# Performance work log

Measured on AMD Instinct MI355X. Metric: run time of the kernel, lower is better.

The kernel has to match this reference:

```python
import jax, jax.numpy as jnp
import numpy as np

ANG = 7; C = 32; H = 32; W = 32; B = 4
E = 4 * C; HEADS = 4; NV = ANG * 32; TOK = C * NV; HID = int(C * 2.66)


def _ln(x, g, b, eps=1e-6):
    m = x.mean(-1, keepdims=True)
    v = ((x - m) ** 2).mean(-1, keepdims=True)
    return (x - m) * jax.lax.rsqrt(v + eps) * g + b


def _ln_nchw(x, g, b):
    return _ln(x.transpose(0, 2, 3, 1), g, b).transpose(0, 3, 1, 2)


def _l2(x):
    return x / jnp.maximum(jnp.linalg.norm(x, axis=-1, keepdims=True), 1e-12)


def _c11(w, x):  # 1x1 conv, w: [out, in]
    return jnp.einsum('oc,bchw->bohw', w, x)


def _dw3(x, w):  # depthwise 3x3, w: [Ch, 1, 3, 3]
    return jax.lax.conv_general_dilated(x, w, (1, 1), ((1, 1), (1, 1)),
                                        dimension_numbers=('NCHW', 'OIHW', 'NCHW'),
                                        feature_group_count=x.shape[1])


def _branch(buf, p):  # buf: [B, C, N, V, W]
    lin_w, temp, ln1_g, ln1_b, qkv_w, qkvdw_w, proj_w, attca_w, lne_g, lne_b, pin_w, dw_w, pout_w = p
    Bb, Cc, N, V, Wd = buf.shape
    L = V * Wd
    x_tok = buf.transpose(0, 3, 4, 1, 2).reshape(Bb, L, Cc * N) @ lin_w.T  # [B, L, E]
    x_res = buf.transpose(0, 2, 1, 3, 4).reshape(Bb * N, Cc, V, Wd)
    x = x_tok.reshape(Bb, V, Wd, E).transpose(0, 3, 1, 2)  # [B, E, V, W]
    qkv = _dw3(_c11(qkv_w, _ln_nchw(x, ln1_g, ln1_b)), qkvdw_w)
    q, k, v_ = jnp.split(qkv, 3, axis=1)
    d = E // HEADS
    to_heads = lambda t: t.reshape(Bb, HEADS, d, L).transpose(0, 1, 3, 2)  # [B, h, L, d]
    q, k, v_ = _l2(to_heads(q)), _l2(to_heads(k)), to_heads(v_)
    logits = jnp.einsum('bhld,bhmd->bhlm', q, k) * temp
    attn0 = jax.nn.softmax(logits, axis=-1)
    a1 = jnp.maximum(logits, 0.0) ** 2
    a1 = jax.nn.gelu(a1, approximate=False) * a1
    scale, shift = jnp.split(jnp.einsum('oh,bhlm->bolm', attca_w, a1), 2, axis=1)
    attn = attn0 * (1.0 + scale) + shift
    out = jnp.einsum('bhlm,bhmd->bhld', attn, v_).transpose(0, 1, 3, 2).reshape(Bb, E, V, Wd)
    out = _c11(proj_w, out).reshape(Bb, Cc, N, V, Wd).transpose(0, 2, 1, 3, 4).reshape(Bb * N, Cc, V, Wd)
    x = x_res + out
    h2 = _dw3(_c11(pin_w, _ln_nchw(x, lne_g, lne_b)), dw_w)
    h1, hg = jnp.split(h2, 2, axis=1)
    x = x + _c11(pout_w, jax.nn.gelu(h1, approximate=False) * hg)
    return x.reshape(Bb, N, Cc, V, Wd).transpose(0, 2, 1, 3, 4)


def _forward(x_lf, hp, vp, f1_w, f2_w):
    Bt = x_lf.shape[0]
    Bb = Bt // (ANG * ANG)
    x6 = x_lf.reshape(Bb, ANG, ANG, C, H, W)  # (b,u,v,c,h,w)
    epi1 = x6.transpose(0, 3, 2, 5, 1, 4).reshape(Bb, C, ANG * W, ANG, H)  # b c (v w) u h
    epi2 = x6.transpose(0, 3, 1, 4, 2, 5).reshape(Bb, C, ANG * H, ANG, W)  # b c (u h) v w
    o1 = _branch(epi1, hp).reshape(Bb, C, ANG, W, ANG, H).transpose(0, 4, 2, 1, 5, 3).reshape(Bt, C, H, W)
    o2 = _branch(epi2, vp).reshape(Bb, C, ANG, H, ANG, W).transpose(0, 2, 4, 1, 3, 5).reshape(Bt, C, H, W)
    g = jnp.concatenate([o1, o2], axis=1).max(axis=(2, 3))  # AdaptiveMaxPool2d(1) -> [Bt, 2C]
    g = g @ f1_w.T
    g = jnp.where(g >= 0, g, 0.1 * g)  # LeakyReLU(0.1)
    g = jax.nn.sigmoid(g @ f2_w.T)[:, :, None, None]
    return o1 * g + o2 * (1.0 - g)


def setup_inputs() -> dict:
    key = jax.random.key(0)
    ks = iter(jax.random.split(key, 64))
    rn = lambda shape: jax.random.normal(next(ks), shape, jnp.float32) * 0.02
    d = {"x_lf": jax.random.normal(next(ks), (B * ANG * ANG, C, H, W), jnp.float32)}
    for pref in ("h_", "v_"):
        d[pref + "lin_w"] = rn((E, TOK))
        d[pref + "temp"] = jnp.ones((1, HEADS, 1, 1), jnp.float32)
        d[pref + "ln1_g"] = jnp.ones((E,), jnp.float32)
        d[pref + "ln1_b"] = jnp.zeros((E,), jnp.float32)
        d[pref + "qkv_w"] = rn((3 * E, E))
        d[pref + "qkvdw_w"] = rn((3 * E, 1, 3, 3))
        d[pref + "proj_w"] = rn((TOK, E))
        d[pref + "attca_w"] = rn((2 * HEADS, HEADS))
        d[pref + "lne_g"] = jnp.ones((C,), jnp.float32)
        d[pref + "lne_b"] = jnp.zeros((C,), jnp.float32)
        d[pref + "pin_w"] = rn((2 * HID, C))
        d[pref + "dw_w"] = rn((2 * HID, 1, 3, 3))
        d[pref + "pout_w"] = rn((C, HID))
    d["f1_w"] = rn((C // 4, 2 * C))
    d["f2_w"] = rn((C, C // 4))
    return d


def reference(x_lf, h_lin_w, h_temp, h_ln1_g, h_ln1_b, h_qkv_w, h_qkvdw_w, h_proj_w, h_attca_w,
              h_lne_g, h_lne_b, h_pin_w, h_dw_w, h_pout_w,
              v_lin_w, v_temp, v_ln1_g, v_ln1_b, v_qkv_w, v_qkvdw_w, v_proj_w, v_attca_w,
              v_lne_g, v_lne_b, v_pin_w, v_dw_w, v_pout_w, f1_w, f2_w):
    hp = (h_lin_w, h_temp, h_ln1_g, h_ln1_b, h_qkv_w, h_qkvdw_w, h_proj_w, h_attca_w,
          h_lne_g, h_lne_b, h_pin_w, h_dw_w, h_pout_w)
    vp = (v_lin_w, v_temp, v_ln1_g, v_ln1_b, v_qkv_w, v_qkvdw_w, v_proj_w, v_attca_w,
          v_lne_g, v_lne_b, v_pin_w, v_dw_w, v_pout_w)
    return _forward(x_lf, hp, vp, f1_w, f2_w)
```

## Files before the change

kernel.cpp:

```cpp
#include <hip/hip_runtime.h>
#include <math.h>

typedef unsigned short u16;
typedef unsigned int   u32;
typedef __attribute__((ext_vector_type(8))) short short8;
typedef __attribute__((ext_vector_type(4))) short short4v;
typedef __attribute__((ext_vector_type(4))) float float4v;
typedef __attribute__((ext_vector_type(2))) float float2v;
typedef __attribute__((ext_vector_type(2))) unsigned int u32x2;

#define DI __device__ __forceinline__

DI float b2f(u16 v){ return __uint_as_float(((u32)v) << 16); }
DI u16 f2b(float f){
  u32 u = __float_as_uint(f);
  u32 r = (u + 0x7fffu + ((u >> 16) & 1u)) >> 16;
  return (u16)r;
}
DI float fast_gelu(float x){
  float ax = fabsf(x) * 0.70710678118654752f;
  float t  = __builtin_amdgcn_rcpf(fmaf(0.3275911f, ax, 1.0f));
  float p  = t * (0.254829592f + t * (-0.284496736f + t * (1.421413741f +
             t * (-1.453152027f + t * 1.061405429f))));
  float e  = __expf(-ax * ax);
  float ea = fmaf(-p, e, 1.0f);
  float er = (x >= 0.f) ? ea : -ea;
  return 0.5f * x * (1.0f + er);
}

DI float2v pk_fma(float2v a, float2v b, float2v c){
  float2v d;
  asm("v_pk_fma_f32 %0, %1, %2, %3" : "=v"(d) : "v"(a), "v"(b), "v"(c));
  return d;
}
DI u32 cvt_pk_bf16(float lo, float hi){
  u32 r;
  asm("v_cvt_pk_bf16_f32 %0, %1, %2" : "=v"(r) : "v"(lo), "v"(hi));
  return r;
}


__global__ __launch_bounds__(256) void k_wprep(const float* __restrict__ lw0,
    const float* __restrict__ lw1, const float* __restrict__ pw0,
    const float* __restrict__ pw1, u16* __restrict__ linwB, u16* __restrict__ projB)
{
  int base = blockIdx.x * 1024 + threadIdx.x;
  #pragma unroll
  for (int r = 0; r < 4; ++r) {
    int i = base + 256 * r;
    if (i < 1835008) {
      const float* src = (i < 917504) ? lw0 : lw1;
      linwB[i] = f2b(src[i % 917504]);
    } else if (i < 3670016) {
      int j = i - 1835008;
      const float* src = (j < 917504) ? pw0 : pw1;
      projB[j] = f2b(src[j % 917504]);
    }
  }
}

__global__ __launch_bounds__(256) void k8w_prep(const float* __restrict__ pin0,
    const float* __restrict__ pin1, const float* __restrict__ po0,
    const float* __restrict__ po1, const float* __restrict__ qw0,
    const float* __restrict__ qw1, u16* __restrict__ pinB, u16* __restrict__ poB,
    u16* __restrict__ qkvwB)
{
  int idx = blockIdx.x * 256 + threadIdx.x;
  if (idx < 12288) {
    int cc = idx & 31;
    int r = (idx >> 5) % 96;
    int hb = (idx >> 5) / 96;
    int br = hb >> 1, half = hb & 1;
    const float* p = br ? pin1 : pin0;
    pinB[idx] = (r < 85) ? f2b(p[(half * 85 + r) * 32 + cc]) : (u16)0;
  } else if (idx < 18432) {
    int j = idx - 12288;
    int r = j % 96;
    int t = j / 96;
    int br = t >> 5, cc = t & 31;
    const float* p = br ? po1 : po0;
    poB[j] = (r < 85) ? f2b(p[cc * 85 + r]) : (u16)0;
  } else if (idx < 116736) {
    int j = idx - 18432;
    int br = j / 49152, rest = j % 49152;
    qkvwB[j] = f2b((br ? qw1 : qw0)[rest]);
  }
}

__global__ __launch_bounds__(256) void k1_mfma(const float* __restrict__ xlf,
    const u16* __restrict__ linwB, float* __restrict__ xqp)
{
  __shared__ __align__(16) u16 Asb[64][40];
  __shared__ __align__(16) u16 Wsb[128][40];
  const int ks   = blockIdx.x;
  const int mblk = blockIdx.y;
  const int bb   = blockIdx.z;
  const int br = bb >> 2, b = bb & 3;
  const int tid = threadIdx.x;
  const int wid = tid >> 6, lane = tid & 63;
  const int quad = lane >> 4, r16 = lane & 15;
  const int m0s = mblk * 64 + wid * 16;
  const bool active = (m0s < 224);
  const u16* wsrc = linwB + br * 917504;
  const int c = ks;

  float4v acc[8];
  #pragma unroll
  for (int nt = 0; nt < 8; ++nt) acc[nt] = (float4v){0.f, 0.f, 0.f, 0.f};

  #pragma unroll 1
  for (int step = 0; step < 7; ++step) {
    const int k0 = ks * 224 + step * 32;
    #pragma unroll
    for (int r = 0; r < 2; ++r) {
      int idx = tid + 256 * r;
      if (br == 0) {
        int ml = idx >> 3, kl4 = idx & 7;
        int l = mblk * 64 + ml;
        float4v v4 = {0.f, 0.f, 0.f, 0.f};
        if (l < 224) {
          int u = l >> 5, h = l & 31;
          v4 = *(const float4v*)&xlf[(b * 49 + u * 7 + step) * 32768 + c * 1024 + h * 32 + kl4 * 4];
        }
        u32 lo = cvt_pk_bf16(v4[0], v4[1]);
        u32 hi = cvt_pk_bf16(v4[2], v4[3]);
        *(u32x2*)&Asb[ml][kl4 * 4] = (u32x2){lo, hi};
      } else {
        int ml4 = idx & 15, kl = idx >> 4;
        int ml0 = ml4 * 4;
        int l0 = mblk * 64 + ml0;
        float4v v4 = {0.f, 0.f, 0.f, 0.f};
        if (l0 < 224) {
          int v2 = l0 >> 5, w2 = l0 & 31;
          v4 = *(const float4v*)&xlf[(b * 49 + step * 7 + v2) * 32768 + c * 1024 + kl * 32 + w2];
        }
        Asb[ml0 + 0][kl] = f2b(v4[0]);
        Asb[ml0 + 1][kl] = f2b(v4[1]);
        Asb[ml0 + 2][kl] = f2b(v4[2]);
        Asb[ml0 + 3][kl] = f2b(v4[3]);
      }
    }
    #pragma unroll
    for (int r = 0; r < 4; ++r) {
      int idx = tid + 256 * r;
      int e = idx >> 3, kl4 = idx & 7;
      *(short4v*)&Wsb[e][kl4 * 4] = *(const short4v*)&wsrc[e * 7168 + k0 + kl4 * 4];
    }
    __syncthreads();
    if (active) {
      short8 af = *(const short8*)&Asb[wid * 16 + r16][quad * 8];
      #pragma unroll
      for (int nt = 0; nt < 8; ++nt) {
        short8 bf = *(const short8*)&Wsb[nt * 16 + r16][quad * 8];
        acc[nt] = __builtin_amdgcn_mfma_f32_16x16x32_bf16(af, bf, acc[nt], 0, 0, 0);
      }
    }
    __syncthreads();
  }
  if (active) {
    float* outp = xqp + ks * 229376 + (bb * 224 + m0s) * 128;
    #pragma unroll
    for (int nt = 0; nt < 8; ++nt) {
      int e = nt * 16 + r16;
      #pragma unroll
      for (int reg = 0; reg < 4; ++reg) {
        int tok = quad * 4 + reg;
        outp[tok * 128 + e] = acc[nt][reg];
      }
    }
  }
}

__global__ __launch_bounds__(256) void k1b_ln(const float* __restrict__ xqp,
    const float* __restrict__ g0, const float* __restrict__ b0,
    const float* __restrict__ g1, const float* __restrict__ b1,
    u16* __restrict__ xn)
{
  const int tid = threadIdx.x;
  const int row = blockIdx.x * 16 + (tid >> 4);
  const int p = tid & 15;
  const int bb = row / 224;
  const int br = bb >> 2;
  const float* lg = br ? g1 : g0;
  const float* lb = br ? b1 : b0;
  const int e0 = p * 8;
  float4v a0 = {0.f,0.f,0.f,0.f}, a1 = {0.f,0.f,0.f,0.f};
  const float* src = xqp + row * 128 + e0;
  #pragma unroll
  for (int ks = 0; ks < 32; ++ks) {
    const float4v* sp = (const float4v*)(src + ks * 229376);
    a0 += sp[0];
    a1 += sp[1];
  }
  float s = 0.f, s2 = 0.f;
  #pragma unroll
  for (int j = 0; j < 4; ++j) {
    s  += a0[j] + a1[j];
    s2 += a0[j] * a0[j] + a1[j] * a1[j];
  }
  #pragma unroll
  for (int m = 8; m >= 1; m >>= 1) {
    s  += __shfl_xor(s, m);
    s2 += __shfl_xor(s2, m);
  }
  float mean = s * (1.f / 128.f);
  float var  = s2 * (1.f / 128.f) - mean * mean;
  float rs   = rsqrtf(fmaxf(var, 0.f) + 1e-6f);
  u16 o[8];
  #pragma unroll
  for (int j = 0; j < 4; ++j) {
    o[j]     = f2b((a0[j] - mean) * rs * lg[e0 + j]     + lb[e0 + j]);
    o[4 + j] = f2b((a1[j] - mean) * rs * lg[e0 + 4 + j] + lb[e0 + 4 + j]);
  }
  *(short8*)&xn[row * 128 + e0] = *(const short8*)o;
}

__global__ __launch_bounds__(256) void k3_mfma(const u16* __restrict__ xn,
    const u16* __restrict__ qkvwB, float* __restrict__ qkvp)
{
  __shared__ u16 xnb[112][140];
  const int mchunk = blockIdx.x;
  const int nh = blockIdx.y;
  const int bb = blockIdx.z;
  const int br = bb >> 2;
  const int tid = threadIdx.x;
  const int wid = tid >> 6, lane = tid & 63;
  const int quad = lane >> 4, r16 = lane & 15;

  #pragma unroll
  for (int i = 0; i < 7; ++i) {
    int idx = tid + 256 * i;
    int row = idx >> 4, c8 = idx & 15;
    *(short8*)&xnb[row][c8 * 8] = *(const short8*)&xn[(bb * 224 + nh * 112 + row) * 128 + c8 * 8];
  }
  __syncthreads();

  const int mtile = mchunk * 64 + wid * 16;
  const u16* wsrc = qkvwB + br * 49152;
  float4v acc[7];
  #pragma unroll
  for (int nt = 0; nt < 7; ++nt) acc[nt] = (float4v){0.f, 0.f, 0.f, 0.f};
  #pragma unroll
  for (int k = 0; k < 4; ++k) {
    short8 af = *(const short8*)&wsrc[(mtile + r16) * 128 + k * 32 + quad * 8];
    #pragma unroll
    for (int nt = 0; nt < 7; ++nt) {
      short8 bf = *(const short8*)&xnb[nt * 16 + r16][k * 32 + quad * 8];
      acc[nt] = __builtin_amdgcn_mfma_f32_16x16x32_bf16(af, bf, acc[nt], 0, 0, 0);
    }
  }
  #pragma unroll
  for (int nt = 0; nt < 7; ++nt) {
    int tok = nh * 112 + nt * 16 + r16;
    #pragma unroll
    for (int reg = 0; reg < 4; ++reg) {
      int o = mtile + quad * 4 + reg;
      qkvp[(bb * 384 + o) * 224 + tok] = acc[nt][reg];
    }
  }
}

__global__ __launch_bounds__(256) void k45_dwheads(const float* __restrict__ qkvp,
    const float* __restrict__ dw0, const float* __restrict__ dw1,
    float* __restrict__ qkvn)
{
  __shared__ float ps[32][161];
  __shared__ float ts[32][137];
  __shared__ float scs[128];
  const int bid = blockIdx.x;
  const int half = bid & 1;
  const int rest = bid >> 1;
  const int h = rest & 3;
  const int sel = (rest >> 2) % 3;
  const int bb = rest / 12;
  const int br = bb >> 2;
  const int tid = threadIdx.x;
  const int o0 = sel * 128 + h * 32;
  const float* src = qkvp + (bb * 384 + o0) * 224;
  const float* dwa = (br ? dw1 : dw0) + o0 * 9;
  const int vin0  = half ? 3 : 0;
  const int nin   = half ? 128 : 160;
  const int vout0 = half ? 4 : 0;
  const int nout  = half ? 96 : 128;
  const int lout0 = vout0 * 32;
  for (int idx = tid; idx < 32 * nin; idx += 256) {
    int d = idx / nin, l = idx - d * nin;
    ps[d][l] = src[d * 224 + vin0 * 32 + l];
  }
  __syncthreads();
  for (int idx = tid; idx < 32 * nout; idx += 256) {
    int d = idx / nout, lo = idx - d * nout;
    int l = lout0 + lo;
    int v = l >> 5, w = l & 31;
    const float* dww = dwa + d * 9;
    float acc = 0.f;
    #pragma unroll
    for (int dy = -1; dy <= 1; ++dy) {
      int vv = v + dy; if (vv < 0 || vv > 6) continue;
      int vloc = vv - vin0;
      #pragma unroll
      for (int dx = -1; dx <= 1; ++dx) {
        int ww = w + dx; if (ww < 0 || ww > 31) continue;
        acc += ps[d][vloc * 32 + ww] * dww[(dy + 1) * 3 + (dx + 1)];
      }
    }
    ts[d][lo] = acc;
  }
  __syncthreads();
  if (tid < nout) {
    float ss = 0.f;
    #pragma unroll 8
    for (int d = 0; d < 32; ++d) { float x = ts[d][tid]; ss += x * x; }
    scs[tid] = (sel < 2) ? (1.0f / fmaxf(sqrtf(ss), 1e-12f)) : 1.0f;
  }
  __syncthreads();
  float* dst = qkvn + ((bb * 3 + sel) * 4 + h) * 7168;
  for (int idx = tid; idx < 32 * nout; idx += 256) {
    int d = idx & 31, lo = idx >> 5;
    dst[(lout0 + lo) * 32 + d] = ts[d][lo] * scs[lo];
  }
}

__global__ __launch_bounds__(256) void k6_attn(const float* __restrict__ qkvn,
    const float* __restrict__ tmp0, const float* __restrict__ tmp1,
    const float* __restrict__ ca0,  const float* __restrict__ ca1,
    u16* __restrict__ aoB)
{
  __shared__ float qs[16][33];
  __shared__ float ks[128][33];
  __shared__ float sS[16 * 228];
  __shared__ float mxs[16], rss[16];
  __shared__ float caf[32], tpf[4];
  const int it = blockIdx.x;
  const int b = blockIdx.y, br = blockIdx.z;
  const int bb = br * 4 + b;
  const int tid = threadIdx.x;
  const float* tw = br ? tmp1 : tmp0;
  const float* cw = br ? ca1 : ca0;
  if (tid < 32) caf[tid] = cw[tid];
  if (tid < 4)  tpf[tid] = tw[tid];
  const int i0 = it * 4;
  const float* qb = qkvn + (bb * 3 + 0) * 4 * 7168;
  const float* kb = qkvn + (bb * 3 + 1) * 4 * 7168;
  const float* vb = qkvn + (bb * 3 + 2) * 4 * 7168;
  #pragma unroll
  for (int r = 0; r < 2; ++r) {
    int idx = tid + 256 * r;
    if (idx < 512) {
      int d = idx & 31, i = (idx >> 5) & 3, h = idx >> 7;
      qs[h * 4 + i][d] = qb[h * 7168 + (i0 + i) * 32 + d];
    }
  }
  __syncthreads();
  const int hC = tid >> 6, iC = (tid >> 4) & 3, jq = tid & 15;
  float qv[32];
  #pragma unroll
  for (int d2 = 0; d2 < 32; ++d2) qv[d2] = qs[hC * 4 + iC][d2];
  for (int jt = 0; jt < 7; ++jt) {
    __syncthreads();
    #pragma unroll
    for (int r = 0; r < 16; ++r) {
      int idx = tid + 256 * r;
      int d = idx & 31, jj = (idx >> 5) & 31, h = idx >> 10;
      ks[h * 32 + jj][d] = kb[h * 7168 + (jt * 32 + jj) * 32 + d];
    }
    __syncthreads();
    float a2[2] = {0.f, 0.f};
    for (int d = 0; d < 32; ++d) {
      #pragma unroll
      for (int r = 0; r < 2; ++r) a2[r] += qv[d] * ks[hC * 32 + jq + 16 * r][d];
    }
    #pragma unroll
    for (int r = 0; r < 2; ++r)
      sS[(hC * 4 + iC) * 228 + jt * 32 + jq + 16 * r] = a2[r] * tpf[hC];
  }
  __syncthreads();
  {
    int p = tid & 15, row = tid >> 4;
    float mx = -1e30f;
    for (int q = 0; q < 14; ++q) mx = fmaxf(mx, sS[row * 228 + p + 16 * q]);
    #pragma unroll
    for (int m = 8; m >= 1; m >>= 1) mx = fmaxf(mx, __shfl_xor(mx, m));
    float es = 0.f;
    for (int q = 0; q < 14; ++q) es += __expf(sS[row * 228 + p + 16 * q] - mx);
    #pragma unroll
    for (int m = 8; m >= 1; m >>= 1) es += __shfl_xor(es, m);
    if (p == 0) { mxs[row] = mx; rss[row] = 1.0f / es; }
  }
  __syncthreads();
  for (int q = 0; q < 4; ++q) {
    int pr = tid + 256 * q;
    if (pr < 896) {
      int i = pr / 224, j = pr % 224;
      float a1[4];
      #pragma unroll
      for (int hh = 0; hh < 4; ++hh) {
        float sv = sS[(hh * 4 + i) * 228 + j];
        float z = fmaxf(sv, 0.f); float z2 = z * z;
        a1[hh] = fast_gelu(z2) * z2;
      }
      #pragma unroll
      for (int hh = 0; hh < 4; ++hh) {
        float sc = 0.f, sh = 0.f;
        #pragma unroll
        for (int k2 = 0; k2 < 4; ++k2) { sc += caf[hh * 4 + k2] * a1[k2]; sh += caf[(hh + 4) * 4 + k2] * a1[k2]; }
        int row = hh * 4 + i;
        float at = __expf(sS[row * 228 + j] - mxs[row]) * rss[row];
        sS[row * 228 + j] = at * (1.f + sc) + sh;
      }
    }
  }
  __syncthreads();
  {
    int d = tid & 31, hpair = (tid >> 5) & 1, rg = tid >> 6;
    float acc[2] = {0.f, 0.f};
    for (int jt = 0; jt < 7; ++jt) {
      __syncthreads();
      #pragma unroll
      for (int r = 0; r < 16; ++r) {
        int idx = tid + 256 * r;
        int dd = idx & 31, jj = (idx >> 5) & 31, hh2 = idx >> 10;
        ks[hh2 * 32 + jj][dd] = vb[hh2 * 7168 + (jt * 32 + jj) * 32 + dd];
      }
      __syncthreads();
      for (int j = 0; j < 32; ++j) {
        #pragma unroll
        for (int c2 = 0; c2 < 2; ++c2) {
          int hh = hpair * 2 + c2;
          acc[c2] += sS[(hh * 4 + rg) * 228 + jt * 32 + j] * ks[hh * 32 + j][d];
        }
      }
    }
    #pragma unroll
    for (int c2 = 0; c2 < 2; ++c2) {
      int hh = hpair * 2 + c2;
      aoB[(bb * 224 + i0 + rg) * 128 + hh * 32 + d] = f2b(acc[c2]);
    }
  }
}

__global__ __launch_bounds__(256) void k7_mfma(const u16* __restrict__ aoB,
    const u16* __restrict__ projB, const float* __restrict__ xlf, u16* __restrict__ x2)
{
  __shared__ u16 Bs[224][140];
  __shared__ float Ts[64][68];
  const int mchunk = blockIdx.x;
  const int mi = blockIdx.y;
  const int bb = blockIdx.z;
  const int br = bb >> 2, b = bb & 3;
  const int tid = threadIdx.x;
  const int wid = tid >> 6, lane = tid & 63;
  const int quad = lane >> 4, r16 = lane & 15;
  const u16* asrc = projB + br * 917504;
  #pragma unroll
  for (int i = 0; i < 14; ++i) {
    int idx = tid + 256 * i;
    int row = idx >> 4, c8 = idx & 15;
    *(short8*)&Bs[row][c8 * 8] = *(const short8*)&aoB[(bb * 224 + row) * 128 + c8 * 8];
  }
  __syncthreads();
  const int mbase = mchunk * 256 + (wid * 4 + mi) * 16;
  float4v acc[14];
  #pragma unroll
  for (int nt = 0; nt < 14; ++nt) acc[nt] = (float4v){0.f, 0.f, 0.f, 0.f};
  #pragma unroll
  for (int k = 0; k < 4; ++k) {
    short8 af = *(const short8*)&asrc[(mbase + r16) * 128 + k * 32 + quad * 8];
    #pragma unroll
    for (int nt = 0; nt < 14; ++nt) {
      short8 bf = *(const short8*)&Bs[nt * 16 + r16][k * 32 + quad * 8];
      acc[nt] = __builtin_amdgcn_mfma_f32_16x16x32_bf16(af, bf, acc[nt], 0, 0, 0);
    }
  }
  #pragma unroll
  for (int rd = 0; rd < 4; ++rd) {
    const int ntn = (rd < 3) ? 4 : 2;
    __syncthreads();
    #pragma unroll
    for (int t = 0; t < 4; ++t) {
      if (t < ntn) {
        #pragma unroll
        for (int reg = 0; reg < 4; ++reg)
          Ts[wid * 16 + quad * 4 + reg][t * 16 + r16] = acc[rd * 4 + t][reg];
      }
    }
    __syncthreads();
    const int nq = ntn * 4;
    #pragma unroll
    for (int pass = 0; pass < 4; ++pass) {
      int idx = tid + 256 * pass;
      if (idx < 64 * nq) {
        int rloc = idx / nq;
        int qc = idx - rloc * nq;
        int row = mchunk * 256 + (((rloc >> 4) * 4 + mi) << 4) + (rloc & 15);
        int c = row / 224, n = row - c * 224;
        int l = rd * 64 + qc * 4;
        float4v tv = *(const float4v*)&Ts[rloc][qc * 4];
        float r0v, r1v, r2v, r3v;
        if (br == 0) {
          int img = b * 49 + (l >> 5) * 7 + (n >> 5);
          const float* xp = xlf + img * 32768 + c * 1024 + (l & 31) * 32 + (n & 31);
          r0v = xp[0]; r1v = xp[32]; r2v = xp[64]; r3v = xp[96];
        } else {
          int img = b * 49 + (n >> 5) * 7 + (l >> 5);
          float4v xv = *(const float4v*)(xlf + img * 32768 + c * 1024 + (n & 31) * 32 + (l & 31));
          r0v = xv[0]; r1v = xv[1]; r2v = xv[2]; r3v = xv[3];
        }
        u32 lo = cvt_pk_bf16(tv[0] + r0v, tv[1] + r1v);
        u32 hi = cvt_pk_bf16(tv[2] + r2v, tv[3] + r3v);
        u16* dp = &x2[(((br * 896 + b * 224 + n) * 32 + c) << 8) + l];
        *(u32x2*)dp = (u32x2){lo, hi};
      }
    }
  }
}

__global__ __launch_bounds__(256, 4) void k8_mfma(u16* x2,
    const float* __restrict__ lg0, const float* __restrict__ lb0,
    const float* __restrict__ lg1, const float* __restrict__ lb1,
    const float* __restrict__ dwa0, const float* __restrict__ dwa1,
    const u16* __restrict__ pinB, const u16* __restrict__ poB)
{
  __shared__ __align__(16) u16 xnb[224][36];
  __shared__ __align__(16) u32 t12[16][231];
  __shared__ __align__(16) u16 gsb[224][20];
  const int img = blockIdx.x;
  const int br  = blockIdx.y;
  const float* lg  = br ? lg1 : lg0;
  const float* lb  = br ? lb1 : lb0;
  const float* dww = br ? dwa1 : dwa0;
  const u16* pinBr = pinB + br * 2 * 96 * 32;
  const u16* poBr  = poB + br * 32 * 96;
  const int tid = threadIdx.x;
  const int wid = tid >> 6, lane = tid & 63;
  const int quad = lane >> 4, r16 = lane & 15;
  u16* src = x2 + (br * 896 + img) * 8192;

  if (tid < 224) {
    float xr[32];
    #pragma unroll
    for (int cc = 0; cc < 32; ++cc) xr[cc] = b2f(src[cc * 256 + tid]);
    float s = 0.f, s2 = 0.f;
    #pragma unroll
    for (int cc = 0; cc < 32; ++cc) { s += xr[cc]; s2 += xr[cc] * xr[cc]; }
    float mean = s * (1.f / 32.f);
    float var  = s2 * (1.f / 32.f) - mean * mean;
    float rs   = rsqrtf(fmaxf(var, 0.f) + 1e-6f);
    #pragma unroll
    for (int cc = 0; cc < 32; ++cc)
      xnb[tid][cc] = f2b((xr[cc] - mean) * rs * lg[cc] + lb[cc]);
  }
  __syncthreads();

  float4v acc[7];
  #pragma unroll
  for (int i = 0; i < 7; ++i) acc[i] = (float4v){0.f, 0.f, 0.f, 0.f};

  #pragma unroll 1
  for (int it = 0; it < 6; ++it) {
    const int r0 = it * 16;
    #pragma unroll
    for (int ni = 0; ni < 4; ++ni) {
      int n = wid + 4 * ni;
      if (n < 14) {
        const int tok = n * 16 + r16;
        short8 bf;
        const u16* xp = &xnb[tok][quad * 8];
        ((short4v*)&bf)[0] = *(const short4v*)xp;
        ((short4v*)&bf)[1] = *(const short4v*)(xp + 4);
        short8 af0 = *(const short8*)&pinBr[((r0 + r16) << 5) + quad * 8];
        short8 af1 = *(const short8*)&pinBr[((96 + r0 + r16) << 5) + quad * 8];
        float4v d0 = __builtin_amdgcn_mfma_f32_16x16x32_bf16(af0, bf,
                       (float4v){0.f, 0.f, 0.f, 0.f}, 0, 0, 0);
        float4v d1 = __builtin_amdgcn_mfma_f32_16x16x32_bf16(af1, bf,
                       (float4v){0.f, 0.f, 0.f, 0.f}, 0, 0, 0);
        const int col = tok + (tok >> 5);
        #pragma unroll
        for (int reg = 0; reg < 4; ++reg)
          t12[quad * 4 + reg][col] = cvt_pk_bf16(d0[reg], d1[reg]);
      }
    }
    if (it > 0) {
      const int koff = (it - 1) * 16;
      #pragma unroll
      for (int i = 0; i < 7; ++i) {
        int u = wid + 4 * i;
        int mt = u / 14, n = u - mt * 14;
        short8 af = {}, bf = {};
        if (quad < 2) {
          af = *(const short8*)&poBr[(mt * 16 + r16) * 96 + koff + quad * 8];
          const u16* gp = &gsb[n * 16 + r16][quad * 8];
          ((short4v*)&bf)[0] = *(const short4v*)gp;
          ((short4v*)&bf)[1] = *(const short4v*)(gp + 4);
        }
        acc[i] = __builtin_amdgcn_mfma_f32_16x16x32_bf16(af, bf, acc[i], 0, 0, 0);
      }
    }
    __syncthreads();
    if (tid < 224) {
      const int rl = tid & 15;
      const int v  = tid >> 5;
      const int wh = (tid >> 4) & 1;
      const int r  = r0 + rl;
      float2v wp[9];
      if (r < 85) {
        const float* w1 = dww + r * 9;
        const float* w2 = dww + (85 + r) * 9;
        #pragma unroll
        for (int t = 0; t < 9; ++t) wp[t] = (float2v){w1[t], w2[t]};
      } else {
        #pragma unroll
        for (int t = 0; t < 9; ++t) wp[t] = (float2v){0.f, 0.f};
      }
      const u32* trow = &t12[rl][0];
      const int c0 = v * 33;
      const int base = wh << 4;
      const bool vok0 = (v > 0), vok2 = (v < 6);
      float2v accP = {0.f, 0.f}, accC = {0.f, 0.f}, accN = {0.f, 0.f};
      #pragma unroll
      for (int it2 = 0; it2 < 18; ++it2) {
        bool cok = true;
        if (it2 == 0)  cok = (wh == 1);
        if (it2 == 17) cok = (wh == 0);
        if (cok) {
          const int cw = base - 1 + it2;
          u32 p0 = vok0 ? trow[c0 - 33 + cw] : 0u;
          u32 p1 =        trow[c0 + cw];
          u32 p2 = vok2 ? trow[c0 + 33 + cw] : 0u;
          float2v x0 = {__uint_as_float(p0 << 16), __uint_as_float(p0 & 0xffff0000u)};
          float2v x1 = {__uint_as_float(p1 << 16), __uint_as_float(p1 & 0xffff0000u)};
          float2v x2v = {__uint_as_float(p2 << 16), __uint_as_float(p2 & 0xffff0000u)};
          accP = pk_fma(x0, wp[2], accP);
          accC = pk_fma(x0, wp[1], accC);
          accN = pk_fma(x0, wp[0], accN);
          accP = pk_fma(x1, wp[5], accP);
          accC = pk_fma(x1, wp[4], accC);
          accN = pk_fma(x1, wp[3], accN);
          accP = pk_fma(x2v, wp[8], accP);
          accC = pk_fma(x2v, wp[7], accC);
          accN = pk_fma(x2v, wp[6], accN);
        }
        if (it2 >= 2) {
          float g = fast_gelu(accP[0]) * accP[1];
          gsb[(v << 5) + base + (it2 - 2)][rl] = f2b(g);
        }
        accP = accC; accC = accN; accN = (float2v){0.f, 0.f};
      }
    }
    __syncthreads();
  }
  {
    const int koff = 80;
    #pragma unroll
    for (int i = 0; i < 7; ++i) {
      int u = wid + 4 * i;
      int mt = u / 14, n = u - mt * 14;
      short8 af = {}, bf = {};
      if (quad < 2) {
        af = *(const short8*)&poBr[(mt * 16 + r16) * 96 + koff + quad * 8];
        const u16* gp = &gsb[n * 16 + r16][quad * 8];
        ((short4v*)&bf)[0] = *(const short4v*)gp;
        ((short4v*)&bf)[1] = *(const short4v*)(gp + 4);
      }
      acc[i] = __builtin_amdgcn_mfma_f32_16x16x32_bf16(af, bf, acc[i], 0, 0, 0);
    }
  }
  #pragma unroll
  for (int i = 0; i < 7; ++i) {
    int u = wid + 4 * i;
    int mt = u / 14, n = u - mt * 14;
    #pragma unroll
    for (int reg = 0; reg < 4; ++reg) {
      int cc = mt * 16 + quad * 4 + reg;
      int tok = n * 16 + r16;
      int o = cc * 256 + tok;
      src[o] = f2b(b2f(src[o]) + acc[i][reg]);
    }
  }
}

__global__ __launch_bounds__(256) void k9_pool(const u16* __restrict__ x3, float* __restrict__ gmax)
{
  __shared__ float red[4];
  const int bid = blockIdx.x;
  const int c64 = bid & 63;
  const int t = bid >> 6;
  const int c = c64 & 31, which = c64 >> 5;
  const int b = t / 49; const int uv = t % 49; const int u = uv / 7; const int vq = uv % 7;
  const int tid = threadIdx.x;
  float mx = -1e30f;
  if (which == 0) {
    int h = tid & 31, w0 = tid >> 5;
    #pragma unroll
    for (int r = 0; r < 4; ++r) {
      int w = w0 + 8 * r;
      mx = fmaxf(mx, b2f(x3[((b * 224 + vq * 32 + w) * 32 + c) * 256 + u * 32 + h]));
    }
  } else {
    int w = tid & 31, h0 = tid >> 5;
    #pragma unroll
    for (int r = 0; r < 4; ++r) {
      int h = h0 + 8 * r;
      mx = fmaxf(mx, b2f(x3[((896 + b * 224 + u * 32 + h) * 32 + c) * 256 + vq * 32 + w]));
    }
  }
  #pragma unroll
  for (int m = 32; m >= 1; m >>= 1) mx = fmaxf(mx, __shfl_xor(mx, m));
  if ((tid & 63) == 0) red[tid >> 6] = mx;
  __syncthreads();
  if (tid == 0)
    gmax[t * 64 + c64] = fmaxf(fmaxf(red[0], red[1]), fmaxf(red[2], red[3]));
}

__global__ __launch_bounds__(256) void k9_fc(const float* __restrict__ gmax,
    const float* __restrict__ f1, const float* __restrict__ f2, float* __restrict__ gate)
{
  int t = blockIdx.x * 256 + threadIdx.x;
  if (t >= 196) return;
  float g1[8];
  #pragma unroll
  for (int o = 0; o < 8; ++o) {
    float a = 0.f;
    #pragma unroll
    for (int c2 = 0; c2 < 64; ++c2) a += f1[o * 64 + c2] * gmax[t * 64 + c2];
    g1[o] = (a >= 0.f) ? a : 0.1f * a;
  }
  #pragma unroll
  for (int c2 = 0; c2 < 32; ++c2) {
    float a = 0.f;
    #pragma unroll
    for (int o = 0; o < 8; ++o) a += f2[c2 * 8 + o] * g1[o];
    gate[t * 32 + c2] = 1.f / (1.f + expf(-a));
  }
}

__global__ __launch_bounds__(256) void k9_final(const u16* __restrict__ x3,
    const float* __restrict__ gate, float* __restrict__ out)
{
  __shared__ float o1s[32][33];
  const int bid = blockIdx.x;
  const int c = bid & 31;
  const int t = bid >> 5;
  const int b = t / 49; const int uv = t % 49; const int u = uv / 7; const int vq = uv % 7;
  const int tid = threadIdx.x;
  const float g = gate[t * 32 + c];
  #pragma unroll
  for (int r = 0; r < 4; ++r) {
    int h = tid & 31; int w = (tid >> 5) + 8 * r;
    o1s[w][h] = b2f(x3[((b * 224 + vq * 32 + w) * 32 + c) * 256 + u * 32 + h]);
  }
  __syncthreads();
  #pragma unroll
  for (int r = 0; r < 4; ++r) {
    int w = tid & 31; int h = (tid >> 5) + 8 * r;
    float o2 = b2f(x3[((896 + b * 224 + u * 32 + h) * 32 + c) * 256 + vq * 32 + w]);
    float o1 = o1s[w][h];
    out[(t * 32 + c) * 1024 + h * 32 + w] = o1 * g + o2 * (1.f - g);
  }
}

extern "C" void kernel_launch(void* const* d_in, const int* in_sizes, int n_in,
                              void* d_out, int out_size, void* d_ws, size_t ws_size,
                              hipStream_t stream)
{
  const float* xlf    = (const float*)d_in[0];
  const float* h_lin  = (const float*)d_in[1];
  const float* h_temp = (const float*)d_in[2];
  const float* h_g1   = (const float*)d_in[3];
  const float* h_b1   = (const float*)d_in[4];
  const float* h_qkv  = (const float*)d_in[5];
  const float* h_qdw  = (const float*)d_in[6];
  const float* h_proj = (const float*)d_in[7];
  const float* h_ca   = (const float*)d_in[8];
  const float* h_ge   = (const float*)d_in[9];
  const float* h_be   = (const float*)d_in[10];
  const float* h_pin  = (const float*)d_in[11];
  const float* h_dw   = (const float*)d_in[12];
  const float* h_po   = (const float*)d_in[13];
  const float* v_lin  = (const float*)d_in[14];
  const float* v_temp = (const float*)d_in[15];
  const float* v_g1   = (const float*)d_in[16];
  const float* v_b1   = (const float*)d_in[17];
  const float* v_qkv  = (const float*)d_in[18];
  const float* v_qdw  = (const float*)d_in[19];
  const float* v_proj = (const float*)d_in[20];
  const float* v_ca   = (const float*)d_in[21];
  const float* v_ge   = (const float*)d_in[22];
  const float* v_be   = (const float*)d_in[23];
  const float* v_pin  = (const float*)d_in[24];
  const float* v_dw   = (const float*)d_in[25];
  const float* v_po   = (const float*)d_in[26];
  const float* f1     = (const float*)d_in[27];
  const float* f2     = (const float*)d_in[28];

  char* w = (char*)d_ws;
  u16*   x2    = (u16*)  (w + 0);
  float* xqp   = (float*)(w + 0);
  float* qkvp  = (float*)(w + 29360128);
  float* qkvn  = (float*)(w + 32112640);
  float* gmax  = (float*)(w + 34865152);
  float* gate  = (float*)(w + 34915328);
  u16*   pinB  = (u16*)  (w + 34940416);
  u16*   poB   = (u16*)  (w + 34964992);
  u16*   qkvwB = (u16*)  (w + 34977280);
  u16*   aoB   = (u16*)  (w + 35173888);
  u16*   linwB = (u16*)  (w + 35632640);
  u16*   projB = (u16*)  (w + 39302656);
  u16*   xn    = (u16*)  (w + 42972672);

  k_wprep  <<<3584, 256, 0, stream>>>(h_lin, v_lin, h_proj, v_proj, linwB, projB);
  k8w_prep <<<456, 256, 0, stream>>>(h_pin, v_pin, h_po, v_po, h_qkv, v_qkv, pinB, poB, qkvwB);
  k1_mfma  <<<dim3(32, 4, 8), 256, 0, stream>>>(xlf, linwB, xqp);
  k1b_ln   <<<112, 256, 0, stream>>>(xqp, h_g1, h_b1, v_g1, v_b1, xn);
  k3_mfma  <<<dim3(6, 2, 8), 256, 0, stream>>>(xn, qkvwB, qkvp);
  k45_dwheads <<<192, 256, 0, stream>>>(qkvp, h_qdw, v_qdw, qkvn);
  k6_attn  <<<dim3(56, 4, 2), 256, 0, stream>>>(qkvn, h_temp, v_temp, h_ca, v_ca, aoB);
  k7_mfma  <<<dim3(28, 4, 8), 256, 0, stream>>>(aoB, projB, xlf, x2);
  k8_mfma  <<<dim3(896, 2), 256, 0, stream>>>(x2, h_ge, h_be, v_ge, v_be,
                                              h_dw, v_dw, pinB, poB);
  k9_pool  <<<12544, 256, 0, stream>>>(x2, gmax);
  k9_fc    <<<1, 256, 0, stream>>>(gmax, f1, f2, gate);
  k9_final <<<6272, 256, 0, stream>>>(x2, gate, (float*)d_out);
}
```

Before: 396.9 us.

## Merge weight-prep kernels, fold gate FC into final kernel, drop LDS staging

Combines the two weight-conversion kernels into a single launch and folds the tiny gate FC kernel into the final blend kernel, so each block computes its own gate. Two launches are removed. In the qkv and projection GEMMs, the shared-memory staging of the B operand is removed and fragments are read directly from global memory, which eliminates a barrier and LDS traffic. The cost is that the FC work is repeated in every final block, and the direct global B reads rely on cache hits instead of reuse from LDS.

```diff
diff --git a/kernel.cpp b/kernel.cpp
--- a/kernel.cpp
+++ b/kernel.cpp
@@ -40,50 +40,50 @@
 }
 
 
-__global__ __launch_bounds__(256) void k_wprep(const float* __restrict__ lw0,
+__global__ __launch_bounds__(256) void k_prep(const float* __restrict__ lw0,
     const float* __restrict__ lw1, const float* __restrict__ pw0,
-    const float* __restrict__ pw1, u16* __restrict__ linwB, u16* __restrict__ projB)
-{
-  int base = blockIdx.x * 1024 + threadIdx.x;
-  #pragma unroll
-  for (int r = 0; r < 4; ++r) {
-    int i = base + 256 * r;
-    if (i < 1835008) {
-      const float* src = (i < 917504) ? lw0 : lw1;
-      linwB[i] = f2b(src[i % 917504]);
-    } else if (i < 3670016) {
-      int j = i - 1835008;
-      const float* src = (j < 917504) ? pw0 : pw1;
-      projB[j] = f2b(src[j % 917504]);
-    }
-  }
-}
-
-__global__ __launch_bounds__(256) void k8w_prep(const float* __restrict__ pin0,
-    const float* __restrict__ pin1, const float* __restrict__ po0,
-    const float* __restrict__ po1, const float* __restrict__ qw0,
-    const float* __restrict__ qw1, u16* __restrict__ pinB, u16* __restrict__ poB,
-    u16* __restrict__ qkvwB)
-{
-  int idx = blockIdx.x * 256 + threadIdx.x;
-  if (idx < 12288) {
-    int cc = idx & 31;
-    int r = (idx >> 5) % 96;
-    int hb = (idx >> 5) / 96;
-    int br = hb >> 1, half = hb & 1;
-    const float* p = br ? pin1 : pin0;
-    pinB[idx] = (r < 85) ? f2b(p[(half * 85 + r) * 32 + cc]) : (u16)0;
-  } else if (idx < 18432) {
-    int j = idx - 12288;
-    int r = j % 96;
-    int t = j / 96;
-    int br = t >> 5, cc = t & 31;
-    const float* p = br ? po1 : po0;
-    poB[j] = (r < 85) ? f2b(p[cc * 85 + r]) : (u16)0;
-  } else if (idx < 116736) {
-    int j = idx - 18432;
-    int br = j / 49152, rest = j % 49152;
-    qkvwB[j] = f2b((br ? qw1 : qw0)[rest]);
+    const float* __restrict__ pw1,
+    const float* __restrict__ pin0, const float* __restrict__ pin1,
+    const float* __restrict__ po0,  const float* __restrict__ po1,
+    const float* __restrict__ qw0,  const float* __restrict__ qw1,
+    u16* __restrict__ linwB, u16* __restrict__ projB,
+    u16* __restrict__ pinB, u16* __restrict__ poB, u16* __restrict__ qkvwB)
+{
+  if (blockIdx.x < 3584) {
+    int base = blockIdx.x * 1024 + threadIdx.x;
+    #pragma unroll
+    for (int r = 0; r < 4; ++r) {
+      int i = base + 256 * r;
+      if (i < 1835008) {
+        const float* src = (i < 917504) ? lw0 : lw1;
+        linwB[i] = f2b(src[i % 917504]);
+      } else if (i < 3670016) {
+        int j = i - 1835008;
+        const float* src = (j < 917504) ? pw0 : pw1;
+        projB[j] = f2b(src[j % 917504]);
+      }
+    }
+  } else {
+    int idx = (blockIdx.x - 3584) * 256 + threadIdx.x;
+    if (idx < 12288) {
+      int cc = idx & 31;
+      int r = (idx >> 5) % 96;
+      int hb = (idx >> 5) / 96;
+      int br = hb >> 1, half = hb & 1;
+      const float* p = br ? pin1 : pin0;
+      pinB[idx] = (r < 85) ? f2b(p[(half * 85 + r) * 32 + cc]) : (u16)0;
+    } else if (idx < 18432) {
+      int j = idx - 12288;
+      int r = j % 96;
+      int t = j / 96;
+      int br = t >> 5, cc = t & 31;
+      const float* p = br ? po1 : po0;
+      poB[j] = (r < 85) ? f2b(p[cc * 85 + r]) : (u16)0;
+    } else if (idx < 116736) {
+      int j = idx - 18432;
+      int br = j / 49152, rest = j % 49152;
+      qkvwB[j] = f2b((br ? qw1 : qw0)[rest]);
+    }
   }
 }
 
@@ -218,7 +218,6 @@
 __global__ __launch_bounds__(256) void k3_mfma(const u16* __restrict__ xn,
     const u16* __restrict__ qkvwB, float* __restrict__ qkvp)
 {
-  __shared__ u16 xnb[112][140];
   const int mchunk = blockIdx.x;
   const int nh = blockIdx.y;
   const int bb = blockIdx.z;
@@ -227,16 +226,9 @@
   const int wid = tid >> 6, lane = tid & 63;
   const int quad = lane >> 4, r16 = lane & 15;
 
-  #pragma unroll
-  for (int i = 0; i < 7; ++i) {
-    int idx = tid + 256 * i;
-    int row = idx >> 4, c8 = idx & 15;
-    *(short8*)&xnb[row][c8 * 8] = *(const short8*)&xn[(bb * 224 + nh * 112 + row) * 128 + c8 * 8];
-  }
-  __syncthreads();
-
   const int mtile = mchunk * 64 + wid * 16;
   const u16* wsrc = qkvwB + br * 49152;
+  const u16* bsrc = xn + (bb * 224 + nh * 112) * 128;
   float4v acc[7];
   #pragma unroll
   for (int nt = 0; nt < 7; ++nt) acc[nt] = (float4v){0.f, 0.f, 0.f, 0.f};
@@ -245,7 +237,7 @@
     short8 af = *(const short8*)&wsrc[(mtile + r16) * 128 + k * 32 + quad * 8];
     #pragma unroll
     for (int nt = 0; nt < 7; ++nt) {
-      short8 bf = *(const short8*)&xnb[nt * 16 + r16][k * 32 + quad * 8];
+      short8 bf = *(const short8*)&bsrc[(nt * 16 + r16) * 128 + k * 32 + quad * 8];
       acc[nt] = __builtin_amdgcn_mfma_f32_16x16x32_bf16(af, bf, acc[nt], 0, 0, 0);
     }
   }
@@ -442,7 +434,6 @@
 __global__ __launch_bounds__(256) void k7_mfma(const u16* __restrict__ aoB,
     const u16* __restrict__ projB, const float* __restrict__ xlf, u16* __restrict__ x2)
 {
-  __shared__ u16 Bs[224][140];
   __shared__ float Ts[64][68];
   const int mchunk = blockIdx.x;
   const int mi = blockIdx.y;
@@ -452,13 +443,7 @@
   const int wid = tid >> 6, lane = tid & 63;
   const int quad = lane >> 4, r16 = lane & 15;
   const u16* asrc = projB + br * 917504;
-  #pragma unroll
-  for (int i = 0; i < 14; ++i) {
-    int idx = tid + 256 * i;
-    int row = idx >> 4, c8 = idx & 15;
-    *(short8*)&Bs[row][c8 * 8] = *(const short8*)&aoB[(bb * 224 + row) * 128 + c8 * 8];
-  }
-  __syncthreads();
+  const u16* bsrc = aoB + bb * 224 * 128;
   const int mbase = mchunk * 256 + (wid * 4 + mi) * 16;
   float4v acc[14];
   #pragma unroll
@@ -468,7 +453,7 @@
     short8 af = *(const short8*)&asrc[(mbase + r16) * 128 + k * 32 + quad * 8];
     #pragma unroll
     for (int nt = 0; nt < 14; ++nt) {
-      short8 bf = *(const short8*)&Bs[nt * 16 + r16][k * 32 + quad * 8];
+      short8 bf = *(const short8*)&bsrc[(nt * 16 + r16) * 128 + k * 32 + quad * 8];
       acc[nt] = __builtin_amdgcn_mfma_f32_16x16x32_bf16(af, bf, acc[nt], 0, 0, 0);
     }
   }
@@ -712,44 +697,37 @@
     gmax[t * 64 + c64] = fmaxf(fmaxf(red[0], red[1]), fmaxf(red[2], red[3]));
 }
 
-__global__ __launch_bounds__(256) void k9_fc(const float* __restrict__ gmax,
-    const float* __restrict__ f1, const float* __restrict__ f2, float* __restrict__ gate)
-{
-  int t = blockIdx.x * 256 + threadIdx.x;
-  if (t >= 196) return;
-  float g1[8];
-  #pragma unroll
-  for (int o = 0; o < 8; ++o) {
-    float a = 0.f;
-    #pragma unroll
-    for (int c2 = 0; c2 < 64; ++c2) a += f1[o * 64 + c2] * gmax[t * 64 + c2];
-    g1[o] = (a >= 0.f) ? a : 0.1f * a;
-  }
-  #pragma unroll
-  for (int c2 = 0; c2 < 32; ++c2) {
-    float a = 0.f;
-    #pragma unroll
-    for (int o = 0; o < 8; ++o) a += f2[c2 * 8 + o] * g1[o];
-    gate[t * 32 + c2] = 1.f / (1.f + expf(-a));
-  }
-}
-
 __global__ __launch_bounds__(256) void k9_final(const u16* __restrict__ x3,
-    const float* __restrict__ gate, float* __restrict__ out)
+    const float* __restrict__ gmax, const float* __restrict__ f1,
+    const float* __restrict__ f2, float* __restrict__ out)
 {
   __shared__ float o1s[32][33];
+  __shared__ float g1s[8];
+  __shared__ float gs;
   const int bid = blockIdx.x;
   const int c = bid & 31;
   const int t = bid >> 5;
   const int b = t / 49; const int uv = t % 49; const int u = uv / 7; const int vq = uv % 7;
   const int tid = threadIdx.x;
-  const float g = gate[t * 32 + c];
   #pragma unroll
   for (int r = 0; r < 4; ++r) {
     int h = tid & 31; int w = (tid >> 5) + 8 * r;
     o1s[w][h] = b2f(x3[((b * 224 + vq * 32 + w) * 32 + c) * 256 + u * 32 + h]);
   }
-  __syncthreads();
+  if (tid < 8) {
+    float a = 0.f;
+    for (int c2 = 0; c2 < 64; ++c2) a += f1[tid * 64 + c2] * gmax[t * 64 + c2];
+    g1s[tid] = (a >= 0.f) ? a : 0.1f * a;
+  }
+  __syncthreads();
+  if (tid == 0) {
+    float a = 0.f;
+    #pragma unroll
+    for (int o = 0; o < 8; ++o) a += f2[c * 8 + o] * g1s[o];
+    gs = 1.f / (1.f + expf(-a));
+  }
+  __syncthreads();
+  const float g = gs;
   #pragma unroll
   for (int r = 0; r < 4; ++r) {
     int w = tid & 31; int h = (tid >> 5) + 8 * r;
@@ -799,7 +777,6 @@
   float* qkvp  = (float*)(w + 29360128);
   float* qkvn  = (float*)(w + 32112640);
   float* gmax  = (float*)(w + 34865152);
-  float* gate  = (float*)(w + 34915328);
   u16*   pinB  = (u16*)  (w + 34940416);
   u16*   poB   = (u16*)  (w + 34964992);
   u16*   qkvwB = (u16*)  (w + 34977280);
@@ -808,8 +785,9 @@
   u16*   projB = (u16*)  (w + 39302656);
   u16*   xn    = (u16*)  (w + 42972672);
 
-  k_wprep  <<<3584, 256, 0, stream>>>(h_lin, v_lin, h_proj, v_proj, linwB, projB);
-  k8w_prep <<<456, 256, 0, stream>>>(h_pin, v_pin, h_po, v_po, h_qkv, v_qkv, pinB, poB, qkvwB);
+  k_prep   <<<4040, 256, 0, stream>>>(h_lin, v_lin, h_proj, v_proj,
+                                      h_pin, v_pin, h_po, v_po, h_qkv, v_qkv,
+                                      linwB, projB, pinB, poB, qkvwB);
   k1_mfma  <<<dim3(32, 4, 8), 256, 0, stream>>>(xlf, linwB, xqp);
   k1b_ln   <<<112, 256, 0, stream>>>(xqp, h_g1, h_b1, v_g1, v_b1, xn);
   k3_mfma  <<<dim3(6, 2, 8), 256, 0, stream>>>(xn, qkvwB, qkvp);
@@ -819,6 +797,5 @@
   k8_mfma  <<<dim3(896, 2), 256, 0, stream>>>(x2, h_ge, h_be, v_ge, v_be,
                                               h_dw, v_dw, pinB, poB);
   k9_pool  <<<12544, 256, 0, stream>>>(x2, gmax);
-  k9_fc    <<<1, 256, 0, stream>>>(gmax, f1, f2, gate);
-  k9_final <<<6272, 256, 0, stream>>>(x2, gate, (float*)d_out);
-}
+  k9_final <<<6272, 256, 0, stream>>>(x2, gmax, f1, f2, (float*)d_out);
+}
```

After: 412.7 us. 4.0% more time.
